# Kernel optimization log

Measured on AMD Instinct MI355X. Metric: run time of the kernel, lower is better.

## Reference

```python
import jax, jax.numpy as jnp
import numpy as np

N_NODES = 100000
N_EDGES = 1600000
IN_FEATS, N_HIDDEN, N_CLASSES = 128, 64, 40


def setup_inputs() -> dict:
    key = jax.random.key(0)
    ks = jax.random.split(key, 6)
    h = jax.random.normal(ks[0], (N_NODES, IN_FEATS), dtype=jnp.float32)
    W0 = jax.random.normal(ks[1], (IN_FEATS, N_HIDDEN), dtype=jnp.float32) * (1.0 / np.sqrt(IN_FEATS))
    b0 = jnp.zeros((N_HIDDEN,), dtype=jnp.float32)
    W1 = jax.random.normal(ks[2], (N_HIDDEN, N_HIDDEN), dtype=jnp.float32) * (1.0 / np.sqrt(N_HIDDEN))
    b1 = jnp.zeros((N_HIDDEN,), dtype=jnp.float32)
    W2 = jax.random.normal(ks[3], (N_HIDDEN, N_CLASSES), dtype=jnp.float32) * (1.0 / np.sqrt(N_HIDDEN))
    b2 = jnp.zeros((N_CLASSES,), dtype=jnp.float32)
    src = jax.random.randint(ks[4], (N_EDGES,), 0, N_NODES, dtype=jnp.int32)
    dst = jax.random.randint(ks[5], (N_EDGES,), 0, N_NODES, dtype=jnp.int32)
    return {"h": h, "W0": W0, "b0": b0, "W1": W1, "b1": b1, "W2": W2, "b2": b2, "src": src, "dst": dst}


def _degrees(src, dst):
    ones = jnp.ones(src.shape[0], dtype=jnp.float32)
    out_deg = jax.ops.segment_sum(ones, src, num_segments=N_NODES)
    in_deg = jax.ops.segment_sum(ones, dst, num_segments=N_NODES)
    # DGL clamps degrees to >= 1 (allow_zero_in_degree)
    norm_src = jax.lax.rsqrt(jnp.maximum(out_deg, 1.0))  # [N]
    norm_dst = jax.lax.rsqrt(jnp.maximum(in_deg, 1.0))   # [N]
    return norm_src, norm_dst


def _graph_conv(x, W, b, src, dst, norm_src, norm_dst, act):
    # DGL GraphConv, norm='both': D_in^{-1/2} A^T D_out^{-1/2} (X W) + b
    xw = (x @ W) * norm_src[:, None]               # [N, out]
    agg = jax.ops.segment_sum(xw[src], dst, num_segments=N_NODES)  # gather-scatter over edges
    out = agg * norm_dst[:, None] + b
    return jax.nn.relu(out) if act else out


def reference(h, W0, b0, W1, b1, W2, b2, src, dst):
    norm_src, norm_dst = _degrees(src, dst)
    h = _graph_conv(h, W0, b0, src, dst, norm_src, norm_dst, act=True)
    # dropout layers are identity at inference
    h = _graph_conv(h, W1, b1, src, dst, norm_src, norm_dst, act=True)
    h = _graph_conv(h, W2, b2, src, dst, norm_src, norm_dst, act=False)
    return h
```

## Files before the change

kernel.cpp:

```cpp
#include <hip/hip_runtime.h>
#include <hip/hip_fp16.h>

#define N_NODES 100000
#define N_EDGES 1600000
#define ELL_W 64
#define ZROW N_NODES
#define NCHUNK 128
#define NSEG 2
#define CH (N_EDGES / NCHUNK)
#define SEGN (N_NODES / NSEG)

typedef _Float16 half8 __attribute__((ext_vector_type(8)));
typedef float floatx4 __attribute__((ext_vector_type(4)));


__global__ __launch_bounds__(512) void k_count(const int* __restrict__ src, const int* __restrict__ dst,
                                               unsigned char* __restrict__ cnt_out,
                                               unsigned char* __restrict__ cnt_in) {
    __shared__ unsigned pkIn[SEGN / 4];
    __shared__ unsigned pkOut[SEGN / 4];
    const int c = blockIdx.x;
    const int lo = blockIdx.y * SEGN;
    for (int i = threadIdx.x; i < SEGN / 4; i += 512) { pkIn[i] = 0; pkOut[i] = 0; }
    __syncthreads();
    const int4* s4 = (const int4*)(src + c * CH);
    const int4* d4 = (const int4*)(dst + c * CH);
    for (int i = threadIdx.x; i < CH / 4; i += 512) {
        int4 s = s4[i], d = d4[i];
        unsigned a;
        a = (unsigned)(s.x - lo); if (a < SEGN) atomicAdd(&pkOut[a >> 2], 1u << ((a & 3) * 8));
        a = (unsigned)(s.y - lo); if (a < SEGN) atomicAdd(&pkOut[a >> 2], 1u << ((a & 3) * 8));
        a = (unsigned)(s.z - lo); if (a < SEGN) atomicAdd(&pkOut[a >> 2], 1u << ((a & 3) * 8));
        a = (unsigned)(s.w - lo); if (a < SEGN) atomicAdd(&pkOut[a >> 2], 1u << ((a & 3) * 8));
        a = (unsigned)(d.x - lo); if (a < SEGN) atomicAdd(&pkIn[a >> 2], 1u << ((a & 3) * 8));
        a = (unsigned)(d.y - lo); if (a < SEGN) atomicAdd(&pkIn[a >> 2], 1u << ((a & 3) * 8));
        a = (unsigned)(d.z - lo); if (a < SEGN) atomicAdd(&pkIn[a >> 2], 1u << ((a & 3) * 8));
        a = (unsigned)(d.w - lo); if (a < SEGN) atomicAdd(&pkIn[a >> 2], 1u << ((a & 3) * 8));
    }
    __syncthreads();
    unsigned* win  = (unsigned*)(cnt_in  + (size_t)c * N_NODES + lo);
    unsigned* wout = (unsigned*)(cnt_out + (size_t)c * N_NODES + lo);
    for (int i = threadIdx.x; i < SEGN / 4; i += 512) { win[i] = pkIn[i]; wout[i] = pkOut[i]; }
}

__global__ __launch_bounds__(256) void k_scan(unsigned char* __restrict__ cnt_in,
                                              const unsigned char* __restrict__ cnt_out,
                                              int* __restrict__ fill, float* __restrict__ norm_src,
                                              float* __restrict__ norm_dst) {
    int d = blockIdx.x * 256 + threadIdx.x;
    if (d >= N_NODES) return;
    int run = 0;
    for (int c = 0; c < NCHUNK; ++c) {
        int v = cnt_in[(size_t)c * N_NODES + d];
        cnt_in[(size_t)c * N_NODES + d] = (unsigned char)run;
        run += v;
    }
    int od = 0;
    for (int c = 0; c < NCHUNK; ++c) od += cnt_out[(size_t)c * N_NODES + d];
    fill[d] = run;
    norm_dst[d] = rsqrtf((float)(run < 1 ? 1 : run));
    norm_src[d] = rsqrtf((float)(od  < 1 ? 1 : od ));
}

__global__ __launch_bounds__(512) void k_scatter(const int* __restrict__ src, const int* __restrict__ dst,
                                                 const unsigned char* __restrict__ bases,
                                                 int* __restrict__ ell) {
    __shared__ unsigned base4[SEGN / 4];
    const int c = blockIdx.x;
    const int lo = blockIdx.y * SEGN;
    const unsigned* bw = (const unsigned*)(bases + (size_t)c * N_NODES + lo);
    for (int i = threadIdx.x; i < SEGN / 4; i += 512) base4[i] = bw[i];
    __syncthreads();
    const int4* s4 = (const int4*)(src + c * CH);
    const int4* d4 = (const int4*)(dst + c * CH);
    for (int i = threadIdx.x; i < CH / 4; i += 512) {
        int4 s = s4[i], d = d4[i];
        unsigned r, sh, old; int p;
        r = (unsigned)(d.x - lo); if (r < SEGN) { sh = (r & 3) * 8; old = atomicAdd(&base4[r >> 2], 1u << sh); p = (old >> sh) & 0xFF; if (p < ELL_W) ell[p * N_NODES + lo + r] = s.x; }
        r = (unsigned)(d.y - lo); if (r < SEGN) { sh = (r & 3) * 8; old = atomicAdd(&base4[r >> 2], 1u << sh); p = (old >> sh) & 0xFF; if (p < ELL_W) ell[p * N_NODES + lo + r] = s.y; }
        r = (unsigned)(d.z - lo); if (r < SEGN) { sh = (r & 3) * 8; old = atomicAdd(&base4[r >> 2], 1u << sh); p = (old >> sh) & 0xFF; if (p < ELL_W) ell[p * N_NODES + lo + r] = s.z; }
        r = (unsigned)(d.w - lo); if (r < SEGN) { sh = (r & 3) * 8; old = atomicAdd(&base4[r >> 2], 1u << sh); p = (old >> sh) & 0xFF; if (p < ELL_W) ell[p * N_NODES + lo + r] = s.w; }
    }
}

__device__ __forceinline__ void acc16B(const float4& v, float* acc) {
    const __half2* hh = (const __half2*)&v;
    #pragma unroll
    for (int t = 0; t < 4; ++t) {
        float2 f = __half22float2(hh[t]);
        acc[2 * t + 0] += f.x;
        acc[2 * t + 1] += f.y;
    }
}

template<int KK>
__device__ __forceinline__ void loadb8(float4* V, const __half* __restrict__ base,
                                       const int* __restrict__ idxr, int b, int q) {
    #pragma unroll
    for (int u = 0; u < 8; ++u)
        V[u] = *(const float4*)(base + (long)idxr[b + u] * KK + q * 8);
}

__device__ __forceinline__ void accb8(const float4* V, float* acc) {
    #pragma unroll
    for (int u = 0; u < 8; ++u) acc16B(V[u], acc);
}

template<int KK>
__device__ __forceinline__ void gather_row(float* acc, const __half* __restrict__ XW,
                                           const int* __restrict__ idxr, int dg, int q) {
    int nb = (dg + 7) >> 3;
    if (nb <= 0) return;
    float4 va[8], vb[8];
    loadb8<KK>(va, XW, idxr, 0, q);
    int it = 1;
    for (; it + 1 < nb; it += 2) {
        loadb8<KK>(vb, XW, idxr, it * 8, q);
        accb8(va, acc);
        loadb8<KK>(va, XW, idxr, (it + 1) * 8, q);
        accb8(vb, acc);
    }
    if (it < nb) {
        loadb8<KK>(vb, XW, idxr, it * 8, q);
        accb8(va, acc);
        accb8(vb, acc);
    } else {
        accb8(va, acc);
    }
}

template<int K, int NCOL>
__global__ __launch_bounds__(256) void k_gemm(const float* __restrict__ Xv, const float* __restrict__ W,
                                              const float* __restrict__ norm, __half* __restrict__ Y,
                                              __half* __restrict__ padB, __half* __restrict__ padC) {
    constexpr int NT = (NCOL + 15) / 16;
    constexpr int NR = NT * 16;
    __shared__ __align__(16) _Float16 Xh[64][K + 8];
    __shared__ __align__(16) _Float16 Wt[NR][K + 8];
    const int tid = threadIdx.x;
    const int row0 = blockIdx.x * 64;

    if (blockIdx.x == 0) {
        if (tid < 32)       { ((unsigned*)(Y    + (size_t)N_NODES * 64))[tid]      = 0u; }
        else if (tid < 64)  { ((unsigned*)(padB + (size_t)N_NODES * 64))[tid - 32] = 0u; }
        else if (tid < 84)  { ((unsigned*)(padC + (size_t)N_NODES * 40))[tid - 64] = 0u; }
    }

    for (int idx = tid; idx < K * NCOL; idx += 256) {
        int k = idx / NCOL, c = idx - (idx / NCOL) * NCOL;
        Wt[c][k] = (_Float16)W[idx];
    }
    for (int idx = tid; idx < (NR - NCOL) * K; idx += 256) {
        int c = NCOL + idx / K, k = idx - (idx / K) * K;
        Wt[c][k] = (_Float16)0;
    }

    for (int idx = tid; idx < 64 * (K / 8); idx += 256) {
        int r = idx / (K / 8), kc = idx - (idx / (K / 8)) * (K / 8);
        int gr = row0 + r;
        half8 v = {0, 0, 0, 0, 0, 0, 0, 0};
        if (gr < N_NODES) {
            const float* X = Xv + (long)gr * K + kc * 8;
            float4 u0 = *(const float4*)(X + 0);
            float4 u1 = *(const float4*)(X + 4);
            v.s0 = (_Float16)u0.x; v.s1 = (_Float16)u0.y;
            v.s2 = (_Float16)u0.z; v.s3 = (_Float16)u0.w;
            v.s4 = (_Float16)u1.x; v.s5 = (_Float16)u1.y;
            v.s6 = (_Float16)u1.z; v.s7 = (_Float16)u1.w;
        }
        *(half8*)&Xh[r][kc * 8] = v;
    }
    __syncthreads();

    const int lane = tid & 63;
    const int wave = tid >> 6;
    const int quad = lane >> 4;
    const int l16 = lane & 15;
    const int r0 = wave * 16;

    floatx4 acc[NT] = {};
    #pragma unroll
    for (int k0 = 0; k0 < K; k0 += 32) {
        half8 a = *(const half8*)&Xh[r0 + l16][k0 + quad * 8];
        #pragma unroll
        for (int t = 0; t < NT; ++t) {
            half8 b = *(const half8*)&Wt[t * 16 + l16][k0 + quad * 8];
            acc[t] = __builtin_amdgcn_mfma_f32_16x16x32_f16(a, b, acc[t], 0, 0, 0);
        }
    }

    #pragma unroll
    for (int i = 0; i < 4; ++i) {
        int gr = row0 + r0 + quad * 4 + i;
        if (gr < N_NODES) {
            float s = norm[gr];
            #pragma unroll
            for (int t = 0; t < NT; ++t) {
                int c = t * 16 + l16;
                if (c < NCOL) Y[(long)gr * NCOL + c] = __float2half(acc[t][i] * s);
            }
        }
    }
}

template<int K, int NCOL>
__global__ __launch_bounds__(512, 4) void k_agg_gemm(const __half* __restrict__ XWp, const int* __restrict__ ell,
                                                     const int* __restrict__ deg, const float* __restrict__ norm_dst,
                                                     const float* __restrict__ biasp, const float* __restrict__ W,
                                                     const float* __restrict__ norm, __half* __restrict__ Y) {
    constexpr int NT = (NCOL + 15) / 16;
    constexpr int NR = NT * 16;
    __shared__ __align__(16) _Float16 Xh[64][K + 8];
    __shared__ __align__(16) _Float16 Wt[NR][K + 8];
    __shared__ int sIdx[64][68];
    __shared__ int sDeg[64];
    __shared__ int sMax;
    const int tid = threadIdx.x;
    const int row0 = blockIdx.x * 64;

    for (int idx = tid; idx < K * NCOL; idx += 512) {
        int k = idx / NCOL, c = idx - (idx / NCOL) * NCOL;
        Wt[c][k] = (_Float16)W[idx];
    }
    for (int idx = tid; idx < (NR - NCOL) * K; idx += 512) {
        int c = NCOL + idx / K, k = idx - (idx / K) * K;
        Wt[c][k] = (_Float16)0;
    }

    if (tid < 64) {
        int node = row0 + tid;
        int dg = 0;
        if (node < N_NODES) { dg = deg[node]; if (dg > ELL_W) dg = ELL_W; }
        sDeg[tid] = dg;
        int v = dg;
        #pragma unroll
        for (int o = 32; o > 0; o >>= 1) v = max(v, __shfl_down(v, o));
        if (tid == 0) sMax = v;
    }
    __syncthreads();
    const int mpad = (sMax + 7) & ~7;
    for (int i = tid; i < mpad * 64; i += 512) {
        int slot = i >> 6, r = i & 63;
        int node = row0 + r;
        sIdx[r][slot] = (node < N_NODES && slot < sDeg[r]) ? ell[slot * N_NODES + node] : ZROW;
    }
    __syncthreads();

    {
        int r = tid >> 3, q = tid & 7;
        int d = row0 + r;
        int dg = sDeg[r];
        const int* idxr = sIdx[r];
        float acc[8] = {};
        gather_row<K>(acc, XWp, idxr, dg, q);
        _Float16 res[8] = {};
        if (d < N_NODES) {
            float nd = norm_dst[d];
            #pragma unroll
            for (int t = 0; t < 8; ++t) {
                float o = acc[t] * nd + biasp[q * 8 + t];
                res[t] = (_Float16)fmaxf(o, 0.f);
            }
        }
        *(half8*)&Xh[r][q * 8] = *(const half8*)res;
    }
    __syncthreads();

    const int lane = tid & 63;
    const int wave = tid >> 6;
    if (wave < 4) {
        const int quad = lane >> 4;
        const int l16 = lane & 15;
        const int r0 = wave * 16;

        floatx4 acc[NT] = {};
        #pragma unroll
        for (int k0 = 0; k0 < K; k0 += 32) {
            half8 a = *(const half8*)&Xh[r0 + l16][k0 + quad * 8];
            #pragma unroll
            for (int t = 0; t < NT; ++t) {
                half8 b = *(const half8*)&Wt[t * 16 + l16][k0 + quad * 8];
                acc[t] = __builtin_amdgcn_mfma_f32_16x16x32_f16(a, b, acc[t], 0, 0, 0);
            }
        }

        #pragma unroll
        for (int i = 0; i < 4; ++i) {
            int gr = row0 + r0 + quad * 4 + i;
            if (gr < N_NODES) {
                float s = norm[gr];
                #pragma unroll
                for (int t = 0; t < NT; ++t) {
                    int c = t * 16 + l16;
                    if (c < NCOL) Y[(long)gr * NCOL + c] = __float2half(acc[t][i] * s);
                }
            }
        }
    }
}

template<int NF>
__global__ __launch_bounds__(320, 4) void k_agg_f(const __half* __restrict__ XW, const int* __restrict__ ell,
                                                  const int* __restrict__ deg, const float* __restrict__ norm_dst,
                                                  const float* __restrict__ bias, float* __restrict__ OUT) {
    constexpr int NQ = NF / 8;
    __shared__ int sIdx[64][68];
    __shared__ int sDeg[64];
    __shared__ int sMax;
    const int tid = threadIdx.x;
    const int row0 = blockIdx.x * 64;

    if (tid < 64) {
        int node = row0 + tid;
        int dg = 0;
        if (node < N_NODES) { dg = deg[node]; if (dg > ELL_W) dg = ELL_W; }
        sDeg[tid] = dg;
        int v = dg;
        #pragma unroll
        for (int o = 32; o > 0; o >>= 1) v = max(v, __shfl_down(v, o));
        if (tid == 0) sMax = v;
    }
    __syncthreads();
    const int mpad = (sMax + 7) & ~7;
    for (int i = tid; i < mpad * 64; i += 320) {
        int slot = i >> 6, r = i & 63;
        int node = row0 + r;
        sIdx[r][slot] = (node < N_NODES && slot < sDeg[r]) ? ell[slot * N_NODES + node] : ZROW;
    }
    __syncthreads();

    const int r = tid / NQ, q = tid - (tid / NQ) * NQ;
    const int d = row0 + r;
    if (d >= N_NODES) return;
    const int dg = sDeg[r];
    const int* idxr = sIdx[r];

    float acc[8] = {};
    gather_row<NF>(acc, XW, idxr, dg, q);

    float nd = norm_dst[d];
    float o[8];
    #pragma unroll
    for (int t = 0; t < 8; ++t) o[t] = acc[t] * nd + bias[q * 8 + t];
    *(float4*)(OUT + (long)d * NF + q * 8 + 0) = make_float4(o[0], o[1], o[2], o[3]);
    *(float4*)(OUT + (long)d * NF + q * 8 + 4) = make_float4(o[4], o[5], o[6], o[7]);
}

extern "C" void kernel_launch(void* const* d_in, const int* in_sizes, int n_in,
                              void* d_out, int out_size, void* d_ws, size_t ws_size,
                              hipStream_t stream) {
    const float* h  = (const float*)d_in[0];
    const float* W0 = (const float*)d_in[1];
    const float* b0 = (const float*)d_in[2];
    const float* W1 = (const float*)d_in[3];
    const float* b1 = (const float*)d_in[4];
    const float* W2 = (const float*)d_in[5];
    const float* b2 = (const float*)d_in[6];
    const int* src  = (const int*)d_in[7];
    const int* dst  = (const int*)d_in[8];
    float* out = (float*)d_out;

    char* ws = (char*)d_ws;
    size_t off = 0;
    int* fill        = (int*)(ws + off); off += (size_t)N_NODES * 4;
    float* norm_src  = (float*)(ws + off); off += (size_t)N_NODES * 4;
    float* norm_dst  = (float*)(ws + off); off += (size_t)N_NODES * 4;
    int* ell         = (int*)(ws + off); off += (size_t)N_NODES * ELL_W * 4;
    unsigned char* cnt_in  = (unsigned char*)(ws + off);
    __half* bufA = (__half*)(ws + off);
    __half* bufC = (__half*)(ws + off + 13000000);
    off += (size_t)NCHUNK * N_NODES;
    unsigned char* cnt_out = (unsigned char*)(ws + off); off += (size_t)NCHUNK * N_NODES;
    __half* bufB  = (__half*)(ws + off); off += (size_t)(N_NODES + 1) * 64 * 2;

    k_count<<<dim3(NCHUNK, NSEG), 512, 0, stream>>>(src, dst, cnt_out, cnt_in);
    k_scan<<<(N_NODES + 255) / 256, 256, 0, stream>>>(cnt_in, cnt_out, fill, norm_src, norm_dst);
    k_scatter<<<dim3(NCHUNK, NSEG), 512, 0, stream>>>(src, dst, cnt_in, ell);

    const int grid = (N_NODES + 63) / 64;

    k_gemm<128, 64><<<grid, 256, 0, stream>>>(h, W0, norm_src, bufA, bufB, bufC);
    k_agg_gemm<64, 64><<<grid, 512, 0, stream>>>(bufA, ell, fill, norm_dst, b0, W1, norm_src, bufB);
    k_agg_gemm<64, 40><<<grid, 512, 0, stream>>>(bufB, ell, fill, norm_dst, b1, W2, norm_src, bufC);
    k_agg_f<40><<<grid, 320, 0, stream>>>(bufC, ell, fill, norm_dst, b2, out);
}
```

Measured before the change: 278.9 us.

## Fuse GEMM and aggregation layers into persistent megakernel with grid barriers

Replaces the four per-layer kernel launches (input GEMM, two aggregate+GEMM, final aggregate) with one persistent kernel of 391 blocks, each processing 4 row tiles per phase and separated by software grid barriers on atomic counters reset in k_count. This removes launch gaps and kernel tail effects between layers. It relies on all 391 blocks being co-resident, since the spin barrier would deadlock otherwise. Each block now also works through its 4 tiles serially, which leaves less parallel slack to hide gather latency.

Measured after the change: 510.1 us. 1.83x slower.

```diff
diff --git a/kernel.cpp b/kernel.cpp
--- a/kernel.cpp
+++ b/kernel.cpp
@@ -9,6 +9,8 @@
 #define NSEG 2
 #define CH (N_EDGES / NCHUNK)
 #define SEGN (N_NODES / NSEG)
+#define MGRID 391
+#define NTILES ((N_NODES + 63) / 64)
 
 typedef _Float16 half8 __attribute__((ext_vector_type(8)));
 typedef float floatx4 __attribute__((ext_vector_type(4)));
@@ -16,11 +18,14 @@
 
 __global__ __launch_bounds__(512) void k_count(const int* __restrict__ src, const int* __restrict__ dst,
                                                unsigned char* __restrict__ cnt_out,
-                                               unsigned char* __restrict__ cnt_in) {
+                                               unsigned char* __restrict__ cnt_in,
+                                               int* __restrict__ bar) {
     __shared__ unsigned pkIn[SEGN / 4];
     __shared__ unsigned pkOut[SEGN / 4];
     const int c = blockIdx.x;
     const int lo = blockIdx.y * SEGN;
+    if (c == 0 && blockIdx.y == 0 && threadIdx.x < 8)
+        __hip_atomic_store(&bar[threadIdx.x], 0, __ATOMIC_RELEASE, __HIP_MEMORY_SCOPE_AGENT);
     for (int i = threadIdx.x; i < SEGN / 4; i += 512) { pkIn[i] = 0; pkOut[i] = 0; }
     __syncthreads();
     const int4* s4 = (const int4*)(src + c * CH);
@@ -129,221 +134,244 @@
     }
 }
 
-template<int K, int NCOL>
-__global__ __launch_bounds__(256) void k_gemm(const float* __restrict__ Xv, const float* __restrict__ W,
-                                              const float* __restrict__ norm, __half* __restrict__ Y,
-                                              __half* __restrict__ padB, __half* __restrict__ padC) {
+__device__ __forceinline__ void gbar(int* __restrict__ bar, int idx) {
+    __syncthreads();
+    if (threadIdx.x == 0) {
+        __threadfence();
+        atomicAdd(&bar[idx], 1);
+        while (__hip_atomic_load(&bar[idx], __ATOMIC_ACQUIRE, __HIP_MEMORY_SCOPE_AGENT) < MGRID)
+            __builtin_amdgcn_s_sleep(8);
+        __threadfence();
+    }
+    __syncthreads();
+}
+
+template<int NCOL>
+__device__ __forceinline__ void agg_layer(char* smem, const __half* __restrict__ XWp,
+                                          const int* __restrict__ ell, const int* __restrict__ deg,
+                                          const float* __restrict__ norm_dst, const float* __restrict__ biasp,
+                                          const float* __restrict__ W, const float* __restrict__ norm,
+                                          __half* __restrict__ Y) {
     constexpr int NT = (NCOL + 15) / 16;
     constexpr int NR = NT * 16;
-    __shared__ __align__(16) _Float16 Xh[64][K + 8];
-    __shared__ __align__(16) _Float16 Wt[NR][K + 8];
+    _Float16 (*Xh)[72] = (_Float16 (*)[72])smem;
+    _Float16 (*Wt)[72] = (_Float16 (*)[72])(smem + 9216);
+    int (*sIdx)[68]    = (int (*)[68])(smem + 18432);
+    int* sDeg          = (int*)(smem + 35840);
+    int* sMax          = (int*)(smem + 36096);
     const int tid = threadIdx.x;
-    const int row0 = blockIdx.x * 64;
-
-    if (blockIdx.x == 0) {
-        if (tid < 32)       { ((unsigned*)(Y    + (size_t)N_NODES * 64))[tid]      = 0u; }
-        else if (tid < 64)  { ((unsigned*)(padB + (size_t)N_NODES * 64))[tid - 32] = 0u; }
-        else if (tid < 84)  { ((unsigned*)(padC + (size_t)N_NODES * 40))[tid - 64] = 0u; }
-    }
-
-    for (int idx = tid; idx < K * NCOL; idx += 256) {
-        int k = idx / NCOL, c = idx - (idx / NCOL) * NCOL;
-        Wt[c][k] = (_Float16)W[idx];
-    }
-    for (int idx = tid; idx < (NR - NCOL) * K; idx += 256) {
-        int c = NCOL + idx / K, k = idx - (idx / K) * K;
-        Wt[c][k] = (_Float16)0;
-    }
-
-    for (int idx = tid; idx < 64 * (K / 8); idx += 256) {
-        int r = idx / (K / 8), kc = idx - (idx / (K / 8)) * (K / 8);
-        int gr = row0 + r;
-        half8 v = {0, 0, 0, 0, 0, 0, 0, 0};
-        if (gr < N_NODES) {
-            const float* X = Xv + (long)gr * K + kc * 8;
-            float4 u0 = *(const float4*)(X + 0);
-            float4 u1 = *(const float4*)(X + 4);
-            v.s0 = (_Float16)u0.x; v.s1 = (_Float16)u0.y;
-            v.s2 = (_Float16)u0.z; v.s3 = (_Float16)u0.w;
-            v.s4 = (_Float16)u1.x; v.s5 = (_Float16)u1.y;
-            v.s6 = (_Float16)u1.z; v.s7 = (_Float16)u1.w;
-        }
-        *(half8*)&Xh[r][kc * 8] = v;
-    }
-    __syncthreads();
-
     const int lane = tid & 63;
     const int wave = tid >> 6;
     const int quad = lane >> 4;
     const int l16 = lane & 15;
-    const int r0 = wave * 16;
-
-    floatx4 acc[NT] = {};
-    #pragma unroll
-    for (int k0 = 0; k0 < K; k0 += 32) {
-        half8 a = *(const half8*)&Xh[r0 + l16][k0 + quad * 8];
-        #pragma unroll
-        for (int t = 0; t < NT; ++t) {
-            half8 b = *(const half8*)&Wt[t * 16 + l16][k0 + quad * 8];
-            acc[t] = __builtin_amdgcn_mfma_f32_16x16x32_f16(a, b, acc[t], 0, 0, 0);
-        }
-    }
-
-    #pragma unroll
-    for (int i = 0; i < 4; ++i) {
-        int gr = row0 + r0 + quad * 4 + i;
-        if (gr < N_NODES) {
-            float s = norm[gr];
-            #pragma unroll
-            for (int t = 0; t < NT; ++t) {
-                int c = t * 16 + l16;
-                if (c < NCOL) Y[(long)gr * NCOL + c] = __float2half(acc[t][i] * s);
-            }
-        }
-    }
-}
-
-template<int K, int NCOL>
-__global__ __launch_bounds__(512, 4) void k_agg_gemm(const __half* __restrict__ XWp, const int* __restrict__ ell,
-                                                     const int* __restrict__ deg, const float* __restrict__ norm_dst,
-                                                     const float* __restrict__ biasp, const float* __restrict__ W,
-                                                     const float* __restrict__ norm, __half* __restrict__ Y) {
-    constexpr int NT = (NCOL + 15) / 16;
-    constexpr int NR = NT * 16;
-    __shared__ __align__(16) _Float16 Xh[64][K + 8];
-    __shared__ __align__(16) _Float16 Wt[NR][K + 8];
-    __shared__ int sIdx[64][68];
-    __shared__ int sDeg[64];
-    __shared__ int sMax;
-    const int tid = threadIdx.x;
-    const int row0 = blockIdx.x * 64;
-
-    for (int idx = tid; idx < K * NCOL; idx += 512) {
+
+    for (int idx = tid; idx < 64 * NCOL; idx += 512) {
         int k = idx / NCOL, c = idx - (idx / NCOL) * NCOL;
         Wt[c][k] = (_Float16)W[idx];
     }
-    for (int idx = tid; idx < (NR - NCOL) * K; idx += 512) {
-        int c = NCOL + idx / K, k = idx - (idx / K) * K;
+    for (int idx = tid; idx < (NR - NCOL) * 64; idx += 512) {
+        int c = NCOL + idx / 64, k = idx & 63;
         Wt[c][k] = (_Float16)0;
     }
 
-    if (tid < 64) {
-        int node = row0 + tid;
-        int dg = 0;
-        if (node < N_NODES) { dg = deg[node]; if (dg > ELL_W) dg = ELL_W; }
-        sDeg[tid] = dg;
-        int v = dg;
-        #pragma unroll
-        for (int o = 32; o > 0; o >>= 1) v = max(v, __shfl_down(v, o));
-        if (tid == 0) sMax = v;
-    }
-    __syncthreads();
-    const int mpad = (sMax + 7) & ~7;
-    for (int i = tid; i < mpad * 64; i += 512) {
-        int slot = i >> 6, r = i & 63;
-        int node = row0 + r;
-        sIdx[r][slot] = (node < N_NODES && slot < sDeg[r]) ? ell[slot * N_NODES + node] : ZROW;
-    }
-    __syncthreads();
-
-    {
-        int r = tid >> 3, q = tid & 7;
-        int d = row0 + r;
-        int dg = sDeg[r];
-        const int* idxr = sIdx[r];
-        float acc[8] = {};
-        gather_row<K>(acc, XWp, idxr, dg, q);
-        _Float16 res[8] = {};
-        if (d < N_NODES) {
-            float nd = norm_dst[d];
-            #pragma unroll
-            for (int t = 0; t < 8; ++t) {
-                float o = acc[t] * nd + biasp[q * 8 + t];
-                res[t] = (_Float16)fmaxf(o, 0.f);
+    for (int tt = 0; tt < 4; ++tt) {
+        int tile = blockIdx.x * 4 + tt;
+        if (tile < NTILES) {
+            const int row0 = tile * 64;
+            __syncthreads();
+            if (tid < 64) {
+                int node = row0 + tid;
+                int dg = 0;
+                if (node < N_NODES) { dg = deg[node]; if (dg > ELL_W) dg = ELL_W; }
+                sDeg[tid] = dg;
+                int v = dg;
+                #pragma unroll
+                for (int o = 32; o > 0; o >>= 1) v = max(v, __shfl_down(v, o));
+                if (tid == 0) *sMax = v;
+            }
+            __syncthreads();
+            const int mpad = (*sMax + 7) & ~7;
+            for (int i = tid; i < mpad * 64; i += 512) {
+                int slot = i >> 6, r = i & 63;
+                int node = row0 + r;
+                sIdx[r][slot] = (node < N_NODES && slot < sDeg[r]) ? ell[slot * N_NODES + node] : ZROW;
+            }
+            __syncthreads();
+            {
+                int r = tid >> 3, q = tid & 7;
+                int d = row0 + r;
+                int dg = sDeg[r];
+                float acc[8] = {};
+                gather_row<64>(acc, XWp, sIdx[r], dg, q);
+                _Float16 res[8] = {};
+                if (d < N_NODES) {
+                    float nd = norm_dst[d];
+                    #pragma unroll
+                    for (int t = 0; t < 8; ++t) {
+                        float o = acc[t] * nd + biasp[q * 8 + t];
+                        res[t] = (_Float16)fmaxf(o, 0.f);
+                    }
+                }
+                *(half8*)&Xh[r][q * 8] = *(const half8*)res;
+            }
+            __syncthreads();
+            if (wave < 4) {
+                const int r0 = wave * 16;
+                floatx4 acc[NT] = {};
+                #pragma unroll
+                for (int k0 = 0; k0 < 64; k0 += 32) {
+                    half8 a = *(const half8*)&Xh[r0 + l16][k0 + quad * 8];
+                    #pragma unroll
+                    for (int t = 0; t < NT; ++t) {
+                        half8 b = *(const half8*)&Wt[t * 16 + l16][k0 + quad * 8];
+                        acc[t] = __builtin_amdgcn_mfma_f32_16x16x32_f16(a, b, acc[t], 0, 0, 0);
+                    }
+                }
+                #pragma unroll
+                for (int i = 0; i < 4; ++i) {
+                    int gr = row0 + r0 + quad * 4 + i;
+                    if (gr < N_NODES) {
+                        float s = norm[gr];
+                        #pragma unroll
+                        for (int t = 0; t < NT; ++t) {
+                            int c = t * 16 + l16;
+                            if (c < NCOL) Y[(long)gr * NCOL + c] = __float2half(acc[t][i] * s);
+                        }
+                    }
+                }
             }
         }
-        *(half8*)&Xh[r][q * 8] = *(const half8*)res;
-    }
-    __syncthreads();
-
+    }
+}
+
+__global__ __launch_bounds__(512, 4) void k_mega(
+        const float* __restrict__ h, const float* __restrict__ W0,
+        const float* __restrict__ norm_src, const float* __restrict__ norm_dst,
+        const int* __restrict__ ell, const int* __restrict__ deg,
+        const float* __restrict__ b0, const float* __restrict__ W1,
+        const float* __restrict__ b1, const float* __restrict__ W2,
+        const float* __restrict__ b2,
+        __half* __restrict__ bufA, __half* __restrict__ bufB, __half* __restrict__ bufC,
+        float* __restrict__ out, int* __restrict__ bar) {
+    __shared__ __align__(16) char smem[36112];
+    const int tid = threadIdx.x;
     const int lane = tid & 63;
     const int wave = tid >> 6;
-    if (wave < 4) {
-        const int quad = lane >> 4;
-        const int l16 = lane & 15;
-        const int r0 = wave * 16;
-
-        floatx4 acc[NT] = {};
-        #pragma unroll
-        for (int k0 = 0; k0 < K; k0 += 32) {
-            half8 a = *(const half8*)&Xh[r0 + l16][k0 + quad * 8];
-            #pragma unroll
-            for (int t = 0; t < NT; ++t) {
-                half8 b = *(const half8*)&Wt[t * 16 + l16][k0 + quad * 8];
-                acc[t] = __builtin_amdgcn_mfma_f32_16x16x32_f16(a, b, acc[t], 0, 0, 0);
-            }
+    const int quad = lane >> 4;
+    const int l16 = lane & 15;
+
+    {
+        _Float16 (*Xh)[136] = (_Float16 (*)[136])smem;
+        _Float16 (*Wt)[136] = (_Float16 (*)[136])(smem + 17408);
+        if (blockIdx.x == 0) {
+            if (tid < 32)      ((unsigned*)(bufA + (size_t)N_NODES * 64))[tid]      = 0u;
+            else if (tid < 64) ((unsigned*)(bufB + (size_t)N_NODES * 64))[tid - 32] = 0u;
+            else if (tid < 84) ((unsigned*)(bufC + (size_t)N_NODES * 40))[tid - 64] = 0u;
         }
-
-        #pragma unroll
-        for (int i = 0; i < 4; ++i) {
-            int gr = row0 + r0 + quad * 4 + i;
-            if (gr < N_NODES) {
-                float s = norm[gr];
-                #pragma unroll
-                for (int t = 0; t < NT; ++t) {
-                    int c = t * 16 + l16;
-                    if (c < NCOL) Y[(long)gr * NCOL + c] = __float2half(acc[t][i] * s);
-                }
-            }
+        for (int idx = tid; idx < 128 * 64; idx += 512) {
+            int k = idx >> 6, c = idx & 63;
+            Wt[c][k] = (_Float16)W0[idx];
         }
-    }
-}
-
-template<int NF>
-__global__ __launch_bounds__(320, 4) void k_agg_f(const __half* __restrict__ XW, const int* __restrict__ ell,
-                                                  const int* __restrict__ deg, const float* __restrict__ norm_dst,
-                                                  const float* __restrict__ bias, float* __restrict__ OUT) {
-    constexpr int NQ = NF / 8;
-    __shared__ int sIdx[64][68];
-    __shared__ int sDeg[64];
-    __shared__ int sMax;
-    const int tid = threadIdx.x;
-    const int row0 = blockIdx.x * 64;
-
-    if (tid < 64) {
-        int node = row0 + tid;
-        int dg = 0;
-        if (node < N_NODES) { dg = deg[node]; if (dg > ELL_W) dg = ELL_W; }
-        sDeg[tid] = dg;
-        int v = dg;
-        #pragma unroll
-        for (int o = 32; o > 0; o >>= 1) v = max(v, __shfl_down(v, o));
-        if (tid == 0) sMax = v;
-    }
-    __syncthreads();
-    const int mpad = (sMax + 7) & ~7;
-    for (int i = tid; i < mpad * 64; i += 320) {
-        int slot = i >> 6, r = i & 63;
-        int node = row0 + r;
-        sIdx[r][slot] = (node < N_NODES && slot < sDeg[r]) ? ell[slot * N_NODES + node] : ZROW;
-    }
-    __syncthreads();
-
-    const int r = tid / NQ, q = tid - (tid / NQ) * NQ;
-    const int d = row0 + r;
-    if (d >= N_NODES) return;
-    const int dg = sDeg[r];
-    const int* idxr = sIdx[r];
-
-    float acc[8] = {};
-    gather_row<NF>(acc, XW, idxr, dg, q);
-
-    float nd = norm_dst[d];
-    float o[8];
-    #pragma unroll
-    for (int t = 0; t < 8; ++t) o[t] = acc[t] * nd + bias[q * 8 + t];
-    *(float4*)(OUT + (long)d * NF + q * 8 + 0) = make_float4(o[0], o[1], o[2], o[3]);
-    *(float4*)(OUT + (long)d * NF + q * 8 + 4) = make_float4(o[4], o[5], o[6], o[7]);
+        for (int tt = 0; tt < 4; ++tt) {
+            int tile = blockIdx.x * 4 + tt;
+            if (tile < NTILES) {
+                const int row0 = tile * 64;
+                __syncthreads();
+                for (int idx = tid; idx < 64 * 16; idx += 512) {
+                    int r = idx >> 4, kc = idx & 15;
+                    int gr = row0 + r;
+                    half8 v = {0, 0, 0, 0, 0, 0, 0, 0};
+                    if (gr < N_NODES) {
+                        const float* X = h + (long)gr * 128 + kc * 8;
+                        float4 u0 = *(const float4*)(X + 0);
+                        float4 u1 = *(const float4*)(X + 4);
+                        v.s0 = (_Float16)u0.x; v.s1 = (_Float16)u0.y;
+                        v.s2 = (_Float16)u0.z; v.s3 = (_Float16)u0.w;
+                        v.s4 = (_Float16)u1.x; v.s5 = (_Float16)u1.y;
+                        v.s6 = (_Float16)u1.z; v.s7 = (_Float16)u1.w;
+                    }
+                    *(half8*)&Xh[r][kc * 8] = v;
+                }
+                __syncthreads();
+                if (wave < 4) {
+                    const int r0 = wave * 16;
+                    floatx4 acc[4] = {};
+                    #pragma unroll
+                    for (int k0 = 0; k0 < 128; k0 += 32) {
+                        half8 a = *(const half8*)&Xh[r0 + l16][k0 + quad * 8];
+                        #pragma unroll
+                        for (int t = 0; t < 4; ++t) {
+                            half8 b = *(const half8*)&Wt[t * 16 + l16][k0 + quad * 8];
+                            acc[t] = __builtin_amdgcn_mfma_f32_16x16x32_f16(a, b, acc[t], 0, 0, 0);
+                        }
+                    }
+                    #pragma unroll
+                    for (int i = 0; i < 4; ++i) {
+                        int gr = row0 + r0 + quad * 4 + i;
+                        if (gr < N_NODES) {
+                            float s = norm_src[gr];
+                            #pragma unroll
+                            for (int t = 0; t < 4; ++t)
+                                bufA[(long)gr * 64 + t * 16 + l16] = __float2half(acc[t][i] * s);
+                        }
+                    }
+                }
+            }
+        }
+    }
+    gbar(bar, 0);
+
+    agg_layer<64>(smem, bufA, ell, deg, norm_dst, b0, W1, norm_src, bufB);
+    gbar(bar, 1);
+
+    agg_layer<40>(smem, bufB, ell, deg, norm_dst, b1, W2, norm_src, bufC);
+    gbar(bar, 2);
+
+    {
+        int (*sIdx)[68] = (int (*)[68])(smem + 18432);
+        int* sDeg       = (int*)(smem + 35840);
+        int* sMax       = (int*)(smem + 36096);
+        for (int tt = 0; tt < 4; ++tt) {
+            int tile = blockIdx.x * 4 + tt;
+            if (tile < NTILES) {
+                const int row0 = tile * 64;
+                __syncthreads();
+                if (tid < 64) {
+                    int node = row0 + tid;
+                    int dg = 0;
+                    if (node < N_NODES) { dg = deg[node]; if (dg > ELL_W) dg = ELL_W; }
+                    sDeg[tid] = dg;
+                    int v = dg;
+                    #pragma unroll
+                    for (int o = 32; o > 0; o >>= 1) v = max(v, __shfl_down(v, o));
+                    if (tid == 0) *sMax = v;
+                }
+                __syncthreads();
+                const int mpad = (*sMax + 7) & ~7;
+                for (int i = tid; i < mpad * 64; i += 512) {
+                    int slot = i >> 6, r = i & 63;
+                    int node = row0 + r;
+                    sIdx[r][slot] = (node < N_NODES && slot < sDeg[r]) ? ell[slot * N_NODES + node] : ZROW;
+                }
+                __syncthreads();
+                if (tid < 320) {
+                    int r = tid / 5, q = tid - (tid / 5) * 5;
+                    int d = row0 + r;
+                    if (d < N_NODES) {
+                        int dg = sDeg[r];
+                        float acc[8] = {};
+                        gather_row<40>(acc, bufC, sIdx[r], dg, q);
+                        float nd = norm_dst[d];
+                        float o[8];
+                        #pragma unroll
+                        for (int t = 0; t < 8; ++t) o[t] = acc[t] * nd + b2[q * 8 + t];
+                        *(float4*)(out + (long)d * 40 + q * 8 + 0) = make_float4(o[0], o[1], o[2], o[3]);
+                        *(float4*)(out + (long)d * 40 + q * 8 + 4) = make_float4(o[4], o[5], o[6], o[7]);
+                    }
+                }
+            }
+        }
+    }
 }
 
 extern "C" void kernel_launch(void* const* d_in, const int* in_sizes, int n_in,
@@ -372,15 +400,12 @@
     off += (size_t)NCHUNK * N_NODES;
     unsigned char* cnt_out = (unsigned char*)(ws + off); off += (size_t)NCHUNK * N_NODES;
     __half* bufB  = (__half*)(ws + off); off += (size_t)(N_NODES + 1) * 64 * 2;
-
-    k_count<<<dim3(NCHUNK, NSEG), 512, 0, stream>>>(src, dst, cnt_out, cnt_in);
+    int* bar      = (int*)(ws + off); off += 256;
+
+    k_count<<<dim3(NCHUNK, NSEG), 512, 0, stream>>>(src, dst, cnt_out, cnt_in, bar);
     k_scan<<<(N_NODES + 255) / 256, 256, 0, stream>>>(cnt_in, cnt_out, fill, norm_src, norm_dst);
     k_scatter<<<dim3(NCHUNK, NSEG), 512, 0, stream>>>(src, dst, cnt_in, ell);
 
-    const int grid = (N_NODES + 63) / 64;
-
-    k_gemm<128, 64><<<grid, 256, 0, stream>>>(h, W0, norm_src, bufA, bufB, bufC);
-    k_agg_gemm<64, 64><<<grid, 512, 0, stream>>>(bufA, ell, fill, norm_dst, b0, W1, norm_src, bufB);
-    k_agg_gemm<64, 40><<<grid, 512, 0, stream>>>(bufB, ell, fill, norm_dst, b1, W2, norm_src, bufC);
-    k_agg_f<40><<<grid, 320, 0, stream>>>(bufC, ell, fill, norm_dst, b2, out);
-}
+    k_mega<<<MGRID, 512, 0, stream>>>(h, W0, norm_src, norm_dst, ell, fill,
+                                      b0, W1, b1, W2, b2, bufA, bufB, bufC, out, bar);
+}
```

## Fuse ELL scatter and first-layer GEMM into one heterogeneous kernel launch

Applied to the files above, without the earlier changes.

Merges the ELL scatter kernel and the first X·W0 GEMM into a single launch, where the first blocks perform the scatter and the remaining blocks compute GEMM tiles. This removes one launch and lets the independent scatter and GEMM work overlap on the GPU. The workspace layout is reshuffled so bufA aliases cnt_out instead of cnt_in, since cnt_in is still read during the scatter, and zeroing of the bufC pad row moves into the first agg_gemm. The fused kernel uses a fixed 50 KB shared buffer and 512-thread blocks, so only 4 of 8 waves do MFMA work in GEMM blocks, and occupancy may be lower than before.

After: 276.0 us. No clear change (-1.0%).

```diff
diff --git a/kernel.cpp b/kernel.cpp
--- a/kernel.cpp
+++ b/kernel.cpp
@@ -9,6 +9,7 @@
 #define NSEG 2
 #define CH (N_EDGES / NCHUNK)
 #define SEGN (N_NODES / NSEG)
+#define NTILES ((N_NODES + 63) / 64)
 
 typedef _Float16 half8 __attribute__((ext_vector_type(8)));
 typedef float floatx4 __attribute__((ext_vector_type(4)));
@@ -62,24 +63,88 @@
     norm_src[d] = rsqrtf((float)(od  < 1 ? 1 : od ));
 }
 
-__global__ __launch_bounds__(512) void k_scatter(const int* __restrict__ src, const int* __restrict__ dst,
-                                                 const unsigned char* __restrict__ bases,
-                                                 int* __restrict__ ell) {
-    __shared__ unsigned base4[SEGN / 4];
-    const int c = blockIdx.x;
-    const int lo = blockIdx.y * SEGN;
-    const unsigned* bw = (const unsigned*)(bases + (size_t)c * N_NODES + lo);
-    for (int i = threadIdx.x; i < SEGN / 4; i += 512) base4[i] = bw[i];
-    __syncthreads();
-    const int4* s4 = (const int4*)(src + c * CH);
-    const int4* d4 = (const int4*)(dst + c * CH);
-    for (int i = threadIdx.x; i < CH / 4; i += 512) {
-        int4 s = s4[i], d = d4[i];
-        unsigned r, sh, old; int p;
-        r = (unsigned)(d.x - lo); if (r < SEGN) { sh = (r & 3) * 8; old = atomicAdd(&base4[r >> 2], 1u << sh); p = (old >> sh) & 0xFF; if (p < ELL_W) ell[p * N_NODES + lo + r] = s.x; }
-        r = (unsigned)(d.y - lo); if (r < SEGN) { sh = (r & 3) * 8; old = atomicAdd(&base4[r >> 2], 1u << sh); p = (old >> sh) & 0xFF; if (p < ELL_W) ell[p * N_NODES + lo + r] = s.y; }
-        r = (unsigned)(d.z - lo); if (r < SEGN) { sh = (r & 3) * 8; old = atomicAdd(&base4[r >> 2], 1u << sh); p = (old >> sh) & 0xFF; if (p < ELL_W) ell[p * N_NODES + lo + r] = s.z; }
-        r = (unsigned)(d.w - lo); if (r < SEGN) { sh = (r & 3) * 8; old = atomicAdd(&base4[r >> 2], 1u << sh); p = (old >> sh) & 0xFF; if (p < ELL_W) ell[p * N_NODES + lo + r] = s.w; }
+__global__ __launch_bounds__(512, 2) void k_scatgemm(const int* __restrict__ src, const int* __restrict__ dst,
+                                                     const unsigned char* __restrict__ bases,
+                                                     int* __restrict__ ell,
+                                                     const float* __restrict__ h, const float* __restrict__ W0,
+                                                     const float* __restrict__ norm_src,
+                                                     __half* __restrict__ bufA, __half* __restrict__ bufB) {
+    __shared__ __align__(16) char smem[50000];
+    const int tid = threadIdx.x;
+
+    if (blockIdx.x < NCHUNK * NSEG) {
+        unsigned* base4 = (unsigned*)smem;
+        const int c = blockIdx.x >> 1;
+        const int lo = (blockIdx.x & 1) * SEGN;
+        const unsigned* bw = (const unsigned*)(bases + (size_t)c * N_NODES + lo);
+        for (int i = tid; i < SEGN / 4; i += 512) base4[i] = bw[i];
+        __syncthreads();
+        const int4* s4 = (const int4*)(src + c * CH);
+        const int4* d4 = (const int4*)(dst + c * CH);
+        for (int i = tid; i < CH / 4; i += 512) {
+            int4 s = s4[i], d = d4[i];
+            unsigned r, sh, old; int p;
+            r = (unsigned)(d.x - lo); if (r < SEGN) { sh = (r & 3) * 8; old = atomicAdd(&base4[r >> 2], 1u << sh); p = (old >> sh) & 0xFF; if (p < ELL_W) ell[p * N_NODES + lo + r] = s.x; }
+            r = (unsigned)(d.y - lo); if (r < SEGN) { sh = (r & 3) * 8; old = atomicAdd(&base4[r >> 2], 1u << sh); p = (old >> sh) & 0xFF; if (p < ELL_W) ell[p * N_NODES + lo + r] = s.y; }
+            r = (unsigned)(d.z - lo); if (r < SEGN) { sh = (r & 3) * 8; old = atomicAdd(&base4[r >> 2], 1u << sh); p = (old >> sh) & 0xFF; if (p < ELL_W) ell[p * N_NODES + lo + r] = s.z; }
+            r = (unsigned)(d.w - lo); if (r < SEGN) { sh = (r & 3) * 8; old = atomicAdd(&base4[r >> 2], 1u << sh); p = (old >> sh) & 0xFF; if (p < ELL_W) ell[p * N_NODES + lo + r] = s.w; }
+        }
+    } else {
+        _Float16 (*Xh)[136] = (_Float16 (*)[136])smem;
+        _Float16 (*Wt)[136] = (_Float16 (*)[136])(smem + 17408);
+        const int tile = blockIdx.x - NCHUNK * NSEG;
+        const int row0 = tile * 64;
+        if (tile == 0) {
+            if (tid < 32)      ((unsigned*)(bufA + (size_t)N_NODES * 64))[tid]      = 0u;
+            else if (tid < 64) ((unsigned*)(bufB + (size_t)N_NODES * 64))[tid - 32] = 0u;
+        }
+        for (int idx = tid; idx < 128 * 64; idx += 512) {
+            int k = idx >> 6, c = idx & 63;
+            Wt[c][k] = (_Float16)W0[idx];
+        }
+        for (int idx = tid; idx < 64 * 16; idx += 512) {
+            int r = idx >> 4, kc = idx & 15;
+            int gr = row0 + r;
+            half8 v = {0, 0, 0, 0, 0, 0, 0, 0};
+            if (gr < N_NODES) {
+                const float* X = h + (long)gr * 128 + kc * 8;
+                float4 u0 = *(const float4*)(X + 0);
+                float4 u1 = *(const float4*)(X + 4);
+                v.s0 = (_Float16)u0.x; v.s1 = (_Float16)u0.y;
+                v.s2 = (_Float16)u0.z; v.s3 = (_Float16)u0.w;
+                v.s4 = (_Float16)u1.x; v.s5 = (_Float16)u1.y;
+                v.s6 = (_Float16)u1.z; v.s7 = (_Float16)u1.w;
+            }
+            *(half8*)&Xh[r][kc * 8] = v;
+        }
+        __syncthreads();
+        const int lane = tid & 63;
+        const int wave = tid >> 6;
+        if (wave < 4) {
+            const int quad = lane >> 4;
+            const int l16 = lane & 15;
+            const int r0 = wave * 16;
+            floatx4 acc[4] = {};
+            #pragma unroll
+            for (int k0 = 0; k0 < 128; k0 += 32) {
+                half8 a = *(const half8*)&Xh[r0 + l16][k0 + quad * 8];
+                #pragma unroll
+                for (int t = 0; t < 4; ++t) {
+                    half8 b = *(const half8*)&Wt[t * 16 + l16][k0 + quad * 8];
+                    acc[t] = __builtin_amdgcn_mfma_f32_16x16x32_f16(a, b, acc[t], 0, 0, 0);
+                }
+            }
+            #pragma unroll
+            for (int i = 0; i < 4; ++i) {
+                int gr = row0 + r0 + quad * 4 + i;
+                if (gr < N_NODES) {
+                    float s = norm_src[gr];
+                    #pragma unroll
+                    for (int t = 0; t < 4; ++t)
+                        bufA[(long)gr * 64 + t * 16 + l16] = __float2half(acc[t][i] * s);
+                }
+            }
+        }
     }
 }
 
@@ -130,84 +195,11 @@
 }
 
 template<int K, int NCOL>
-__global__ __launch_bounds__(256) void k_gemm(const float* __restrict__ Xv, const float* __restrict__ W,
-                                              const float* __restrict__ norm, __half* __restrict__ Y,
-                                              __half* __restrict__ padB, __half* __restrict__ padC) {
-    constexpr int NT = (NCOL + 15) / 16;
-    constexpr int NR = NT * 16;
-    __shared__ __align__(16) _Float16 Xh[64][K + 8];
-    __shared__ __align__(16) _Float16 Wt[NR][K + 8];
-    const int tid = threadIdx.x;
-    const int row0 = blockIdx.x * 64;
-
-    if (blockIdx.x == 0) {
-        if (tid < 32)       { ((unsigned*)(Y    + (size_t)N_NODES * 64))[tid]      = 0u; }
-        else if (tid < 64)  { ((unsigned*)(padB + (size_t)N_NODES * 64))[tid - 32] = 0u; }
-        else if (tid < 84)  { ((unsigned*)(padC + (size_t)N_NODES * 40))[tid - 64] = 0u; }
-    }
-
-    for (int idx = tid; idx < K * NCOL; idx += 256) {
-        int k = idx / NCOL, c = idx - (idx / NCOL) * NCOL;
-        Wt[c][k] = (_Float16)W[idx];
-    }
-    for (int idx = tid; idx < (NR - NCOL) * K; idx += 256) {
-        int c = NCOL + idx / K, k = idx - (idx / K) * K;
-        Wt[c][k] = (_Float16)0;
-    }
-
-    for (int idx = tid; idx < 64 * (K / 8); idx += 256) {
-        int r = idx / (K / 8), kc = idx - (idx / (K / 8)) * (K / 8);
-        int gr = row0 + r;
-        half8 v = {0, 0, 0, 0, 0, 0, 0, 0};
-        if (gr < N_NODES) {
-            const float* X = Xv + (long)gr * K + kc * 8;
-            float4 u0 = *(const float4*)(X + 0);
-            float4 u1 = *(const float4*)(X + 4);
-            v.s0 = (_Float16)u0.x; v.s1 = (_Float16)u0.y;
-            v.s2 = (_Float16)u0.z; v.s3 = (_Float16)u0.w;
-            v.s4 = (_Float16)u1.x; v.s5 = (_Float16)u1.y;
-            v.s6 = (_Float16)u1.z; v.s7 = (_Float16)u1.w;
-        }
-        *(half8*)&Xh[r][kc * 8] = v;
-    }
-    __syncthreads();
-
-    const int lane = tid & 63;
-    const int wave = tid >> 6;
-    const int quad = lane >> 4;
-    const int l16 = lane & 15;
-    const int r0 = wave * 16;
-
-    floatx4 acc[NT] = {};
-    #pragma unroll
-    for (int k0 = 0; k0 < K; k0 += 32) {
-        half8 a = *(const half8*)&Xh[r0 + l16][k0 + quad * 8];
-        #pragma unroll
-        for (int t = 0; t < NT; ++t) {
-            half8 b = *(const half8*)&Wt[t * 16 + l16][k0 + quad * 8];
-            acc[t] = __builtin_amdgcn_mfma_f32_16x16x32_f16(a, b, acc[t], 0, 0, 0);
-        }
-    }
-
-    #pragma unroll
-    for (int i = 0; i < 4; ++i) {
-        int gr = row0 + r0 + quad * 4 + i;
-        if (gr < N_NODES) {
-            float s = norm[gr];
-            #pragma unroll
-            for (int t = 0; t < NT; ++t) {
-                int c = t * 16 + l16;
-                if (c < NCOL) Y[(long)gr * NCOL + c] = __float2half(acc[t][i] * s);
-            }
-        }
-    }
-}
-
-template<int K, int NCOL>
 __global__ __launch_bounds__(512, 4) void k_agg_gemm(const __half* __restrict__ XWp, const int* __restrict__ ell,
                                                      const int* __restrict__ deg, const float* __restrict__ norm_dst,
                                                      const float* __restrict__ biasp, const float* __restrict__ W,
-                                                     const float* __restrict__ norm, __half* __restrict__ Y) {
+                                                     const float* __restrict__ norm, __half* __restrict__ Y,
+                                                     __half* __restrict__ padC) {
     constexpr int NT = (NCOL + 15) / 16;
     constexpr int NR = NT * 16;
     __shared__ __align__(16) _Float16 Xh[64][K + 8];
@@ -217,6 +209,9 @@
     __shared__ int sMax;
     const int tid = threadIdx.x;
     const int row0 = blockIdx.x * 64;
+
+    if (padC && blockIdx.x == 0 && tid < 20)
+        ((unsigned*)(padC + (size_t)N_NODES * 40))[tid] = 0u;
 
     for (int idx = tid; idx < K * NCOL; idx += 512) {
         int k = idx / NCOL, c = idx - (idx / NCOL) * NCOL;
@@ -367,20 +362,20 @@
     float* norm_dst  = (float*)(ws + off); off += (size_t)N_NODES * 4;
     int* ell         = (int*)(ws + off); off += (size_t)N_NODES * ELL_W * 4;
     unsigned char* cnt_in  = (unsigned char*)(ws + off);
+    __half* bufC = (__half*)(ws + off);
+    off += (size_t)NCHUNK * N_NODES;
+    unsigned char* cnt_out = (unsigned char*)(ws + off);
     __half* bufA = (__half*)(ws + off);
-    __half* bufC = (__half*)(ws + off + 13000000);
-    off += (size_t)NCHUNK * N_NODES;
-    unsigned char* cnt_out = (unsigned char*)(ws + off); off += (size_t)NCHUNK * N_NODES;
+    off += (size_t)NCHUNK * N_NODES + 256;
     __half* bufB  = (__half*)(ws + off); off += (size_t)(N_NODES + 1) * 64 * 2;
 
     k_count<<<dim3(NCHUNK, NSEG), 512, 0, stream>>>(src, dst, cnt_out, cnt_in);
     k_scan<<<(N_NODES + 255) / 256, 256, 0, stream>>>(cnt_in, cnt_out, fill, norm_src, norm_dst);
-    k_scatter<<<dim3(NCHUNK, NSEG), 512, 0, stream>>>(src, dst, cnt_in, ell);
-
-    const int grid = (N_NODES + 63) / 64;
-
-    k_gemm<128, 64><<<grid, 256, 0, stream>>>(h, W0, norm_src, bufA, bufB, bufC);
-    k_agg_gemm<64, 64><<<grid, 512, 0, stream>>>(bufA, ell, fill, norm_dst, b0, W1, norm_src, bufB);
-    k_agg_gemm<64, 40><<<grid, 512, 0, stream>>>(bufB, ell, fill, norm_dst, b1, W2, norm_src, bufC);
+    k_scatgemm<<<NCHUNK * NSEG + NTILES, 512, 0, stream>>>(src, dst, cnt_in, ell,
+                                                           h, W0, norm_src, bufA, bufB);
+
+    const int grid = NTILES;
+    k_agg_gemm<64, 64><<<grid, 512, 0, stream>>>(bufA, ell, fill, norm_dst, b0, W1, norm_src, bufB, bufC);
+    k_agg_gemm<64, 40><<<grid, 512, 0, stream>>>(bufB, ell, fill, norm_dst, b1, W2, norm_src, bufC, (__half*)0);
     k_agg_f<40><<<grid, 320, 0, stream>>>(bufC, ell, fill, norm_dst, b2, out);
 }
```
